# Kernel optimization log

Hardware: AMD Instinct MI355X
Metric: run time of the kernel (lower is better)

The kernel has to match this reference:

```python
import jax, jax.numpy as jnp
import numpy as np

H = 16  # hidden_size
I = 30  # GRU input_size (hard-coded in module)


def setup_inputs() -> dict:
    key = jax.random.key(0)
    ks = jax.random.split(key, 12)
    B, T = 4096, 512
    s = lambda k, sh: jax.random.normal(k, sh, jnp.float32) * 0.1
    return {
        "x": jax.random.normal(ks[0], (B, T, I), jnp.float32),
        "lengths": jax.random.randint(ks[1], (B,), 1, T + 1),  # valid lengths in [1, T]
        "w_ih": s(ks[2], (3 * H, I)),
        "w_hh": s(ks[3], (3 * H, H)),
        "b_ih": s(ks[4], (3 * H,)),
        "b_hh": s(ks[5], (3 * H,)),
        "fc1_w": s(ks[6], (H, H)), "fc1_b": s(ks[7], (H,)),
        "fc2_w": s(ks[8], (H, H)), "fc2_b": s(ks[9], (H,)),
        "fc3_w": s(ks[10], (H, H)), "fc3_b": s(ks[11], (H,)),
    }


def _gru_last_hidden(x, lengths, w_ih, w_hh, b_ih, b_hh):
    """Run GRU over padded [B,T,I] and return hidden at t = lengths-1 per row.
    Equivalent to pack_padded -> GRU -> pad_packed -> gather output[b, len-1],
    since h_t only depends on steps <= t."""
    B, T, _ = x.shape
    # Precompute input-side gate activations for all steps: [B,T,3H]
    xg = jnp.einsum('bti,gi->btg', x, w_ih) + b_ih
    xr, xz, xn = jnp.split(xg, 3, axis=-1)
    w_hr, w_hz, w_hn = jnp.split(w_hh, 3, axis=0)
    b_hr, b_hz, b_hn = jnp.split(b_hh, 3)
    tidx = lengths - 1  # [B]

    def step(carry, inp):
        h, last = carry
        t, xr_t, xz_t, xn_t = inp
        r = jax.nn.sigmoid(xr_t + h @ w_hr.T + b_hr)
        z = jax.nn.sigmoid(xz_t + h @ w_hz.T + b_hz)
        n = jnp.tanh(xn_t + r * (h @ w_hn.T + b_hn))
        h = (1.0 - z) * n + z * h
        last = jnp.where((tidx == t)[:, None], h, last)  # capture h at final valid step
        return (h, last), None

    h0 = jnp.zeros((B, H), x.dtype)
    (_, last), _ = jax.lax.scan(
        step, (h0, h0),
        (jnp.arange(T),
         xr.transpose(1, 0, 2), xz.transpose(1, 0, 2), xn.transpose(1, 0, 2)))
    return last  # [B,H]


def reference(x, lengths, w_ih, w_hh, b_ih, b_hh,
              fc1_w, fc1_b, fc2_w, fc2_b, fc3_w, fc3_b):
    h = _gru_last_hidden(x, lengths, w_ih, w_hh, b_ih, b_hh)
    e = h @ fc1_w.T + fc1_b
    e = jax.nn.relu(e) @ fc2_w.T + fc2_b   # dropout is identity in eval mode
    e = jax.nn.relu(e) @ fc3_w.T + fc3_b
    return e
```

## Files before the change

kernel.cpp:

```cpp
#include <hip/hip_runtime.h>
#include <cstdint>
#include <cstddef>

typedef float v2f __attribute__((ext_vector_type(2)));

#define HID 16
#define IN  30

#define FAST_RCP(x) __builtin_amdgcn_rcpf(x)

__device__ __forceinline__ float bperm(int baddr, float v) {
    return __int_as_float(__builtin_amdgcn_ds_bpermute(baddr, __float_as_int(v)));
}
__device__ __forceinline__ float dq1(float v) {
    return __int_as_float(__builtin_amdgcn_mov_dpp(__float_as_int(v), 0xB1, 0xF, 0xF, true));
}
__device__ __forceinline__ float dq2(float v) {
    return __int_as_float(__builtin_amdgcn_mov_dpp(__float_as_int(v), 0x4E, 0xF, 0xF, true));
}
#define PKFMA(acc, a, b) asm("v_pk_fma_f32 %0, %1, %2, %0" : "+v"(acc) : "v"(a), "v"(b))

typedef __attribute__((address_space(3))) unsigned int       lds_u32_t;
typedef const __attribute__((address_space(1))) unsigned int glb_u32_t;
#define GLOAD_LDS(gp, lp) \
    __builtin_amdgcn_global_load_lds((glb_u32_t*)(gp), (lds_u32_t*)(lp), 4, 0, 0)

__global__ void k_hist(const int* __restrict__ len, int* __restrict__ hist, int B, int T) {
    int i = blockIdx.x * 256 + threadIdx.x;
    if (i < B) atomicAdd(hist + (T - len[i]), 1);
}
__global__ __launch_bounds__(512) void k_scan(const int* __restrict__ hist, int* __restrict__ off) {
    __shared__ int s[512];
    int t = threadIdx.x;
    int v = hist[t];
    s[t] = v; __syncthreads();
    int acc = v;
    for (int o = 1; o < 512; o <<= 1) {
        int add = (t >= o) ? s[t - o] : 0;
        __syncthreads();
        acc += add; s[t] = acc;
        __syncthreads();
    }
    off[t] = acc - v;
}
__global__ void k_scatter(const int* __restrict__ len, int* __restrict__ off,
                          int* __restrict__ perm, int B, int T) {
    int i = blockIdx.x * 256 + threadIdx.x;
    if (i < B) {
        int b = T - len[i];
        int p = atomicAdd(off + b, 1);
        perm[p] = i;
    }
}

__global__ __launch_bounds__(512, 4) void gru_enc_kernel(
    const float* __restrict__ x, const int* __restrict__ lengths,
    const float* __restrict__ w_ih, const float* __restrict__ w_hh,
    const float* __restrict__ b_ih, const float* __restrict__ b_hh,
    const float* __restrict__ fc1w, const float* __restrict__ fc1b,
    const float* __restrict__ fc2w, const float* __restrict__ fc2b,
    const float* __restrict__ fc3w, const float* __restrict__ fc3b,
    float* __restrict__ out, const int* __restrict__ perm,
    int B, int T, int nblk)
{
    __shared__ __align__(16) float lds[8][1024];

    const int lane = threadIdx.x & 63;
    const int wib  = threadIdx.x >> 6;
    const int q    = lane & 3;
    const int j    = lane >> 2;

    int pos;
    if (wib < 4) pos = 4 * blockIdx.x + wib;
    else         pos = B - 1 - (4 * blockIdx.x + (wib - 4));
    if (pos < 0 || pos >= B) return;
    if (wib >= 4 && pos < 4 * nblk) return;

    const int row = perm ? perm[pos] : pos;
    const int len = lengths[row];

    const float L2E = 1.4426950408889634f;
    const float gsc[3] = { -L2E, -L2E, 2.0f * L2E };

    v2f wih2[3][4];
#pragma unroll
    for (int g = 0; g < 3; ++g) {
        const float* wr = w_ih + (size_t)(g * HID + j) * IN;
#pragma unroll
        for (int m = 0; m < 4; ++m) {
            int p0 = q * 8 + 2 * m;
            v2f t;
            t.x = (p0     < IN) ? wr[p0]     * gsc[g] : 0.0f;
            t.y = (p0 + 1 < IN) ? wr[p0 + 1] * gsc[g] : 0.0f;
            wih2[g][m] = t;
        }
    }
    v2f whh2[3][2];
#pragma unroll
    for (int g = 0; g < 3; ++g)
#pragma unroll
        for (int m = 0; m < 2; ++m) {
            const float* wr = w_hh + (size_t)(g * HID + j) * HID + q * 4 + 2 * m;
            v2f t; t.x = wr[0] * gsc[g]; t.y = wr[1] * gsc[g];
            whh2[g][m] = t;
        }

    v2f initR; initR.x = q ? 0.0f : -L2E * (b_ih[j] + b_hh[j]);               initR.y = 0.0f;
    v2f initZ; initZ.x = q ? 0.0f : -L2E * (b_ih[HID + j] + b_hh[HID + j]);   initZ.y = 0.0f;
    v2f initN; initN.x = q ? 0.0f : 2.0f * L2E * b_ih[2 * HID + j];           initN.y = 0.0f;
    v2f initH; initH.x = q ? 0.0f : 2.0f * L2E * b_hh[2 * HID + j];           initH.y = 0.0f;

    const int word  = min(lane & 31, 29);
    const int sstep = lane >> 5;
    const float* xrow = x + (size_t)row * T * IN;
    const int tcap = T - 1;

    float* ldsw = &lds[wib][0];
    const float* ldsr = ldsw + q * 8;

    int ba[4];
#pragma unroll
    for (int m = 0; m < 4; ++m) ba[m] = (16 * q + 4 * m) << 2;

#define STAGE(cc) do {                                                     \
        const int t0_ = (cc) << 3;                                         \
        float* lb_ = ldsw + (((cc) & 3) << 8);                             \
        _Pragma("unroll")                                                  \
        for (int i_ = 0; i_ < 4; ++i_) {                                   \
            int ts_ = min(t0_ + (i_ << 1) + sstep, tcap);                  \
            GLOAD_LDS(xrow + (size_t)ts_ * IN + word, lb_ + (i_ << 6));    \
        }                                                                  \
    } while (0)

#define STEP(cw, s) do {                                                    \
        float4 xa_ = *(const float4*)((cw) + ((s) << 5));                   \
        float4 xb_ = *(const float4*)((cw) + ((s) << 5) + 4);               \
        v2f xv[4];                                                          \
        xv[0].x = xa_.x; xv[0].y = xa_.y; xv[1].x = xa_.z; xv[1].y = xa_.w; \
        xv[2].x = xb_.x; xv[2].y = xb_.y; xv[3].x = xb_.z; xv[3].y = xb_.w; \
        v2f ar = initR, az = initZ, an = initN, hn = initH;                 \
        _Pragma("unroll")                                                   \
        for (int m_ = 0; m_ < 4; ++m_) {                                    \
            PKFMA(ar, wih2[0][m_], xv[m_]);                                 \
            PKFMA(az, wih2[1][m_], xv[m_]);                                 \
            PKFMA(an, wih2[2][m_], xv[m_]);                                 \
        }                                                                   \
        _Pragma("unroll")                                                   \
        for (int m_ = 0; m_ < 2; ++m_) {                                    \
            PKFMA(ar, whh2[0][m_], hb2[m_]);                                \
            PKFMA(az, whh2[1][m_], hb2[m_]);                                \
            PKFMA(hn, whh2[2][m_], hb2[m_]);                                \
        }                                                                   \
        float pr  = ar.x + ar.y;  pr  += dq1(pr);  pr  += dq2(pr);          \
        float pz  = az.x + az.y;  pz  += dq1(pz);  pz  += dq2(pz);          \
        float pxn = an.x + an.y;  pxn += dq1(pxn); pxn += dq2(pxn);         \
        float phn = hn.x + hn.y;  phn += dq1(phn); phn += dq2(phn);         \
        float rg = FAST_RCP(1.0f + __builtin_exp2f(pr));                    \
        float zg = FAST_RCP(1.0f + __builtin_exp2f(pz));                    \
        float yy = fmaf(rg, phn, pxn);                                      \
        float ng = fmaf(-2.0f, FAST_RCP(1.0f + __builtin_exp2f(yy)), 1.0f); \
        h_own = fmaf(zg, h_own - ng, ng);                                   \
        float b0 = bperm(ba[0], h_own), b1 = bperm(ba[1], h_own);           \
        float b2 = bperm(ba[2], h_own), b3 = bperm(ba[3], h_own);           \
        hb2[0].x = b0; hb2[0].y = b1; hb2[1].x = b2; hb2[1].y = b3;         \
    } while (0)

    v2f hb2[2];
    hb2[0].x = 0.0f; hb2[0].y = 0.0f; hb2[1].x = 0.0f; hb2[1].y = 0.0f;
    float h_own = 0.0f;

    const int nch = (len + 7) >> 3;

    STAGE(0); STAGE(1); STAGE(2);

    for (int c = 0; c < nch; ++c) {
        asm volatile("s_waitcnt vmcnt(8)" ::: "memory");
        STAGE(c + 3);
        const float* cw = ldsr + ((c & 3) << 8);
        const int nst = min(8, len - (c << 3));
#pragma unroll
        for (int s = 0; s < 8; ++s) {
            if (s >= nst) break;
            STEP(cw, s);
        }
    }

    float hv[16];
#pragma unroll
    for (int k = 0; k < 16; ++k) hv[k] = __shfl(h_own, 4 * k, 64);

    float e1 = fc1b[j];
#pragma unroll
    for (int k = 0; k < 16; ++k) e1 = fmaf(fc1w[j * HID + k], hv[k], e1);

    float v1[16];
#pragma unroll
    for (int k = 0; k < 16; ++k) v1[k] = fmaxf(__shfl(e1, 4 * k, 64), 0.0f);

    float e2 = fc2b[j];
#pragma unroll
    for (int k = 0; k < 16; ++k) e2 = fmaf(fc2w[j * HID + k], v1[k], e2);

    float v2a[16];
#pragma unroll
    for (int k = 0; k < 16; ++k) v2a[k] = fmaxf(__shfl(e2, 4 * k, 64), 0.0f);

    float e3 = fc3b[j];
#pragma unroll
    for (int k = 0; k < 16; ++k) e3 = fmaf(fc3w[j * HID + k], v2a[k], e3);

    if (q == 0) out[(size_t)row * HID + j] = e3;
}

extern "C" void kernel_launch(void* const* d_in, const int* in_sizes, int n_in,
                              void* d_out, int out_size, void* d_ws, size_t ws_size,
                              hipStream_t stream) {
    const float* x    = (const float*)d_in[0];
    const int*   lens = (const int*)d_in[1];
    const float* w_ih = (const float*)d_in[2];
    const float* w_hh = (const float*)d_in[3];
    const float* b_ih = (const float*)d_in[4];
    const float* b_hh = (const float*)d_in[5];
    const float* fc1w = (const float*)d_in[6];
    const float* fc1b = (const float*)d_in[7];
    const float* fc2w = (const float*)d_in[8];
    const float* fc2b = (const float*)d_in[9];
    const float* fc3w = (const float*)d_in[10];
    const float* fc3b = (const float*)d_in[11];
    float* out = (float*)d_out;

    const int B = in_sizes[1];
    const int T = (int)(in_sizes[0] / ((size_t)B * IN));

    int* wsI = (int*)d_ws;
    const size_t need = ((size_t)B + 1024) * sizeof(int);
    const bool dosort = (ws_size >= need) && (T <= 512) && (T >= 8);
    int* perm = dosort ? wsI : nullptr;
    int* hist = wsI + B;
    int* off  = wsI + B + 512;

    if (dosort) {
        hipMemsetAsync(hist, 0, 512 * sizeof(int), stream);
        k_hist<<<(B + 255) / 256, 256, 0, stream>>>(lens, hist, B, T);
        k_scan<<<1, 512, 0, stream>>>(hist, off);
        k_scatter<<<(B + 255) / 256, 256, 0, stream>>>(lens, off, perm, B, T);
    }

    const int nblk = (B + 7) / 8;
    gru_enc_kernel<<<nblk, 512, 0, stream>>>(x, lens, w_ih, w_hh, b_ih, b_hh,
                                             fc1w, fc1b, fc2w, fc2b, fc3w, fc3b,
                                             out, perm, B, T, nblk);
}
```

Measured before the change: 167.5 us.

## Shrink blocks to four waves, drop paired scheduling, split full/remainder chunk loops

The launch changes from 512-thread blocks that pair a short and a long sequence in one block to 256-thread blocks with one sequence per wave, and the LDS array halves to match. Bias initialisation moves out of the packed accumulators and is added after the quad reduction, so each step starts with v_pk_mul instead of a copy plus FMA. The step loop is split into an unconditional 8-step body for full chunks and a guarded remainder tail, which removes the per-step break checks. The intent is to cut per-step instruction overhead and to stop short sequences' waves from sitting idle in a block held by a long partner, at the cost of giving up the explicit load-balancing pairing.

```diff
diff --git a/kernel.cpp b/kernel.cpp
--- a/kernel.cpp
+++ b/kernel.cpp
@@ -19,6 +19,7 @@
     return __int_as_float(__builtin_amdgcn_mov_dpp(__float_as_int(v), 0x4E, 0xF, 0xF, true));
 }
 #define PKFMA(acc, a, b) asm("v_pk_fma_f32 %0, %1, %2, %0" : "+v"(acc) : "v"(a), "v"(b))
+#define PKMUL(d, a, b)   asm("v_pk_mul_f32 %0, %1, %2"     : "=v"(d)   : "v"(a), "v"(b))
 
 typedef __attribute__((address_space(3))) unsigned int       lds_u32_t;
 typedef const __attribute__((address_space(1))) unsigned int glb_u32_t;
@@ -53,7 +54,7 @@
     }
 }
 
-__global__ __launch_bounds__(512, 4) void gru_enc_kernel(
+__global__ __launch_bounds__(256, 4) void gru_enc_kernel(
     const float* __restrict__ x, const int* __restrict__ lengths,
     const float* __restrict__ w_ih, const float* __restrict__ w_hh,
     const float* __restrict__ b_ih, const float* __restrict__ b_hh,
@@ -61,20 +62,17 @@
     const float* __restrict__ fc2w, const float* __restrict__ fc2b,
     const float* __restrict__ fc3w, const float* __restrict__ fc3b,
     float* __restrict__ out, const int* __restrict__ perm,
-    int B, int T, int nblk)
+    int B, int T)
 {
-    __shared__ __align__(16) float lds[8][1024];
+    __shared__ __align__(16) float lds[4][1024];
 
     const int lane = threadIdx.x & 63;
     const int wib  = threadIdx.x >> 6;
     const int q    = lane & 3;
     const int j    = lane >> 2;
 
-    int pos;
-    if (wib < 4) pos = 4 * blockIdx.x + wib;
-    else         pos = B - 1 - (4 * blockIdx.x + (wib - 4));
-    if (pos < 0 || pos >= B) return;
-    if (wib >= 4 && pos < 4 * nblk) return;
+    const int pos = blockIdx.x * 4 + wib;
+    if (pos >= B) return;
 
     const int row = perm ? perm[pos] : pos;
     const int len = lengths[row];
@@ -105,10 +103,10 @@
             whh2[g][m] = t;
         }
 
-    v2f initR; initR.x = q ? 0.0f : -L2E * (b_ih[j] + b_hh[j]);               initR.y = 0.0f;
-    v2f initZ; initZ.x = q ? 0.0f : -L2E * (b_ih[HID + j] + b_hh[HID + j]);   initZ.y = 0.0f;
-    v2f initN; initN.x = q ? 0.0f : 2.0f * L2E * b_ih[2 * HID + j];           initN.y = 0.0f;
-    v2f initH; initH.x = q ? 0.0f : 2.0f * L2E * b_hh[2 * HID + j];           initH.y = 0.0f;
+    const float bR  = -L2E * (b_ih[j] + b_hh[j]);
+    const float bZ  = -L2E * (b_ih[HID + j] + b_hh[HID + j]);
+    const float biN = 2.0f * L2E * b_ih[2 * HID + j];
+    const float bhN = 2.0f * L2E * b_hh[2 * HID + j];
 
     const int word  = min(lane & 31, 29);
     const int sstep = lane >> 5;
@@ -133,54 +131,59 @@
     } while (0)
 
 #define STEP(cw, s) do {                                                    \
-        float4 xa_ = *(const float4*)((cw) + ((s) << 5));                   \
-        float4 xb_ = *(const float4*)((cw) + ((s) << 5) + 4);               \
-        v2f xv[4];                                                          \
-        xv[0].x = xa_.x; xv[0].y = xa_.y; xv[1].x = xa_.z; xv[1].y = xa_.w; \
-        xv[2].x = xb_.x; xv[2].y = xb_.y; xv[3].x = xb_.z; xv[3].y = xb_.w; \
-        v2f ar = initR, az = initZ, an = initN, hn = initH;                 \
-        _Pragma("unroll")                                                   \
-        for (int m_ = 0; m_ < 4; ++m_) {                                    \
-            PKFMA(ar, wih2[0][m_], xv[m_]);                                 \
-            PKFMA(az, wih2[1][m_], xv[m_]);                                 \
-            PKFMA(an, wih2[2][m_], xv[m_]);                                 \
-        }                                                                   \
-        _Pragma("unroll")                                                   \
-        for (int m_ = 0; m_ < 2; ++m_) {                                    \
-            PKFMA(ar, whh2[0][m_], hb2[m_]);                                \
-            PKFMA(az, whh2[1][m_], hb2[m_]);                                \
-            PKFMA(hn, whh2[2][m_], hb2[m_]);                                \
-        }                                                                   \
+        v2f xv0 = *(const v2f*)((cw) + ((s) << 5));                         \
+        v2f xv1 = *(const v2f*)((cw) + ((s) << 5) + 2);                     \
+        v2f xv2 = *(const v2f*)((cw) + ((s) << 5) + 4);                     \
+        v2f xv3 = *(const v2f*)((cw) + ((s) << 5) + 6);                     \
+        v2f ar, az, an, hn;                                                 \
+        PKMUL(ar, wih2[0][0], xv0);                                         \
+        PKMUL(az, wih2[1][0], xv0);                                         \
+        PKMUL(an, wih2[2][0], xv0);                                         \
+        PKFMA(ar, wih2[0][1], xv1); PKFMA(az, wih2[1][1], xv1);             \
+        PKFMA(an, wih2[2][1], xv1);                                         \
+        PKFMA(ar, wih2[0][2], xv2); PKFMA(az, wih2[1][2], xv2);             \
+        PKFMA(an, wih2[2][2], xv2);                                         \
+        PKFMA(ar, wih2[0][3], xv3); PKFMA(az, wih2[1][3], xv3);             \
+        PKFMA(an, wih2[2][3], xv3);                                         \
+        PKMUL(hn, whh2[2][0], hb2[0]); PKFMA(hn, whh2[2][1], hb2[1]);       \
+        PKFMA(ar, whh2[0][0], hb2[0]); PKFMA(ar, whh2[0][1], hb2[1]);       \
+        PKFMA(az, whh2[1][0], hb2[0]); PKFMA(az, whh2[1][1], hb2[1]);       \
         float pr  = ar.x + ar.y;  pr  += dq1(pr);  pr  += dq2(pr);          \
         float pz  = az.x + az.y;  pz  += dq1(pz);  pz  += dq2(pz);          \
         float pxn = an.x + an.y;  pxn += dq1(pxn); pxn += dq2(pxn);         \
         float phn = hn.x + hn.y;  phn += dq1(phn); phn += dq2(phn);         \
-        float rg = FAST_RCP(1.0f + __builtin_exp2f(pr));                    \
-        float zg = FAST_RCP(1.0f + __builtin_exp2f(pz));                    \
-        float yy = fmaf(rg, phn, pxn);                                      \
+        float rg = FAST_RCP(1.0f + __builtin_exp2f(pr + bR));               \
+        float zg = FAST_RCP(1.0f + __builtin_exp2f(pz + bZ));               \
+        float yy = fmaf(rg, phn + bhN, pxn + biN);                          \
         float ng = fmaf(-2.0f, FAST_RCP(1.0f + __builtin_exp2f(yy)), 1.0f); \
         h_own = fmaf(zg, h_own - ng, ng);                                   \
-        float b0 = bperm(ba[0], h_own), b1 = bperm(ba[1], h_own);           \
-        float b2 = bperm(ba[2], h_own), b3 = bperm(ba[3], h_own);           \
-        hb2[0].x = b0; hb2[0].y = b1; hb2[1].x = b2; hb2[1].y = b3;         \
+        hb2[0].x = bperm(ba[0], h_own); hb2[0].y = bperm(ba[1], h_own);     \
+        hb2[1].x = bperm(ba[2], h_own); hb2[1].y = bperm(ba[3], h_own);     \
     } while (0)
 
     v2f hb2[2];
     hb2[0].x = 0.0f; hb2[0].y = 0.0f; hb2[1].x = 0.0f; hb2[1].y = 0.0f;
     float h_own = 0.0f;
 
-    const int nch = (len + 7) >> 3;
+    const int nfull = len >> 3;
+    const int rem   = len & 7;
 
     STAGE(0); STAGE(1); STAGE(2);
 
-    for (int c = 0; c < nch; ++c) {
+    int c = 0;
+    for (; c < nfull; ++c) {
         asm volatile("s_waitcnt vmcnt(8)" ::: "memory");
         STAGE(c + 3);
         const float* cw = ldsr + ((c & 3) << 8);
-        const int nst = min(8, len - (c << 3));
+        STEP(cw, 0); STEP(cw, 1); STEP(cw, 2); STEP(cw, 3);
+        STEP(cw, 4); STEP(cw, 5); STEP(cw, 6); STEP(cw, 7);
+    }
+    if (rem) {
+        asm volatile("s_waitcnt vmcnt(8)" ::: "memory");
+        const float* cw = ldsr + ((c & 3) << 8);
 #pragma unroll
         for (int s = 0; s < 8; ++s) {
-            if (s >= nst) break;
+            if (s >= rem) break;
             STEP(cw, s);
         }
     }
@@ -246,8 +249,8 @@
         k_scatter<<<(B + 255) / 256, 256, 0, stream>>>(lens, off, perm, B, T);
     }
 
-    const int nblk = (B + 7) / 8;
-    gru_enc_kernel<<<nblk, 512, 0, stream>>>(x, lens, w_ih, w_hh, b_ih, b_hh,
+    const int nblk = (B + 3) / 4;
+    gru_enc_kernel<<<nblk, 256, 0, stream>>>(x, lens, w_ih, w_hh, b_ih, b_hh,
                                              fc1w, fc1b, fc2w, fc2b, fc3w, fc3b,
-                                             out, perm, B, T, nblk);
-}
+                                             out, perm, B, T);
+}
```

Result: slower. 173.1 us (+3.4%).
